# Kernel tuning notes

Hardware: AMD Instinct MI355X
Metric: run time of the kernel (lower is better)

The kernel has to match this reference:

```python
import jax, jax.numpy as jnp
import numpy as np
import math

D_MODEL = 512
N_HEADS = 8
KSIZE = 3
SEQ = 2048
BATCH = 4


def setup_inputs() -> dict:
    key = jax.random.key(0)
    ks = jax.random.split(key, 12)
    f32 = jnp.float32
    scale_in = 1.0 / math.sqrt(D_MODEL)
    inp = {
        "query": jax.random.normal(ks[0], (SEQ, BATCH, D_MODEL), f32),
        "key": jax.random.normal(ks[1], (SEQ, BATCH, D_MODEL), f32),
        "value": jax.random.normal(ks[2], (SEQ, BATCH, D_MODEL), f32),
        # causal mask: 1 where attention allowed (lower triangular), 0 elsewhere
        "attn_mask": jnp.tril(jnp.ones((SEQ, SEQ), jnp.int32)),
        "conv1_w": jax.random.normal(ks[3], (D_MODEL, D_MODEL, KSIZE), f32) * scale_in,
        "conv1_b": jax.random.normal(ks[4], (D_MODEL,), f32) * 0.01,
        "conv2_w": jax.random.normal(ks[5], (D_MODEL, D_MODEL, KSIZE), f32) * scale_in,
        "conv2_b": jax.random.normal(ks[6], (D_MODEL,), f32) * 0.01,
        "lin1_w": jax.random.normal(ks[7], (D_MODEL, D_MODEL), f32) * scale_in,
        "lin1_b": jax.random.normal(ks[8], (D_MODEL,), f32) * 0.01,
        "lin2_w": jax.random.normal(ks[9], (D_MODEL, D_MODEL), f32) * scale_in,
        "lin2_b": jax.random.normal(ks[10], (D_MODEL,), f32) * 0.01,
    }
    return inp


def _causal_conv1d(x, w, b):
    # x: [B, S, C_in]; w: [C_out, C_in, K] (torch Conv1d layout); left-pad K-1 (causal)
    K = w.shape[-1]
    xc = jnp.transpose(x, (0, 2, 1))  # [B, C, S]
    y = jax.lax.conv_general_dilated(
        xc, w, window_strides=(1,), padding=[(K - 1, 0)],
        dimension_numbers=("NCH", "OIH", "NCH"))
    y = y + b[None, :, None]
    return jnp.transpose(y, (0, 2, 1))  # [B, S, C_out]


def reference(query, key, value, attn_mask,
              conv1_w, conv1_b, conv2_w, conv2_b,
              lin1_w, lin1_b, lin2_w, lin2_b):
    h, dk = N_HEADS, D_MODEL // N_HEADS
    S, B, D = query.shape
    q = jnp.transpose(query, (1, 0, 2))  # [B, S, D]
    k = jnp.transpose(key, (1, 0, 2))
    v = jnp.transpose(value, (1, 0, 2))

    q = _causal_conv1d(q, conv1_w, conv1_b).reshape(B, S, h, dk).transpose(0, 2, 1, 3)
    k = _causal_conv1d(k, conv2_w, conv2_b).reshape(B, S, h, dk).transpose(0, 2, 1, 3)
    v = (v @ lin1_w.T + lin1_b).reshape(B, S, h, dk).transpose(0, 2, 1, 3)

    scores = jnp.einsum("bhqd,bhkd->bhqk", q, k) / math.sqrt(dk)
    scores = jnp.where(attn_mask[None, None, :, :] == 0, jnp.float32(-1e9), scores)
    p_attn = jax.nn.softmax(scores, axis=-1)  # dropout p=0.0 (deterministic)
    x = jnp.einsum("bhqk,bhkd->bhqd", p_attn, v)
    x = x.transpose(0, 2, 1, 3).reshape(B, S, D)
    out = x @ lin2_w.T + lin2_b
    return jnp.transpose(out, (1, 0, 2))  # back to [S, B, D]
```

## Files before the change

kernel.cpp:

```cpp
#include <hip/hip_runtime.h>
#include <hip/hip_bf16.h>

#define S_LEN 2048
#define BATCH 4
#define DMODEL 512
#define NHEADS 8
#define DK 64
#define NELEM 4194304
#define WSLOT 786432

typedef __hip_bfloat16 bf16;
typedef unsigned short u16_t;
typedef __attribute__((ext_vector_type(8))) short bfx8;
typedef __attribute__((ext_vector_type(4))) short bfx4;
typedef __attribute__((ext_vector_type(4))) float fx4;

#define MFMA16(a, b, c) __builtin_amdgcn_mfma_f32_16x16x32_bf16(a, b, c, 0, 0, 0)

__device__ __forceinline__ float cvt(float x) { return x; }
__device__ __forceinline__ float cvt(bf16 x) { return __bfloat162float(x); }
__device__ __forceinline__ u16_t f2b(float x) { bf16 h = __float2bfloat16(x); return *(u16_t*)&h; }
__device__ __forceinline__ float b2f16(u16_t u) { bf16 h = *(bf16*)&u; return __bfloat162float(h); }

__global__ void sniff_kernel(const u16_t* __restrict__ q, int* __restrict__ flag) {
    const int lane = threadIdx.x & 63;
    int cnt = 0;
    for (int j = 0; j < 4; j++) {
        int e = (q[2 * (lane + 64 * j)] >> 7) & 0xFF;
        cnt += (int)__popcll(__ballot(e >= 100 && e <= 140));
    }
    if (lane == 0 && blockIdx.x == 0) *flag = (cnt >= 200) ? 1 : 0;
}

__global__ void cvt_in_kernel(const void* __restrict__ q, const void* __restrict__ k,
                              const void* __restrict__ v, u16_t* __restrict__ am,
                              const int* __restrict__ flag) {
    int gid = blockIdx.x * 256 + threadIdx.x;
    int e8 = gid * 8;
    int z = e8 >> 22;
    int off = e8 & (NELEM - 1);
    const void* src = (z == 0) ? q : (z == 1) ? k : v;
    u16_t* dst = am + (size_t)z * NELEM + off;
    if (*flag) {
        *(bfx8*)dst = *(const bfx8*)((const u16_t*)src + off);
    } else {
        const float* s = (const float*)src + off;
        fx4 a = *(const fx4*)s;
        fx4 b = *(const fx4*)(s + 4);
        u16_t tmp[8];
#pragma unroll
        for (int j = 0; j < 4; j++) { tmp[j] = f2b(a[j]); tmp[4 + j] = f2b(b[j]); }
        *(bfx8*)dst = *(const bfx8*)tmp;
    }
}

__global__ void cvt_w_kernel(const void* __restrict__ c1w, const void* __restrict__ c2w,
                             const void* __restrict__ l1w, const void* __restrict__ l2w,
                             const void* __restrict__ b0, const void* __restrict__ b1,
                             const void* __restrict__ b2, const void* __restrict__ b3,
                             u16_t* __restrict__ wt, u16_t* __restrict__ bb,
                             const int* __restrict__ flag) {
    const int isbf = *flag;
    if (blockIdx.x >= 3072) {
        int i = (blockIdx.x - 3072) * 256 + threadIdx.x;
        int p = i >> 9, o = i & 511;
        const void* b = (p == 0) ? b0 : (p == 1) ? b1 : (p == 2) ? b2 : b3;
        bb[i] = f2b(isbf ? cvt(((const bf16*)b)[o]) : ((const float*)b)[o]);
        return;
    }
    int gid = blockIdx.x * 256 + threadIdx.x;
    int e4 = gid * 4;
    int p = e4 / WSLOT;
    int r = e4 - p * WSLOT;
    int t = r >> 18;
    int rem = r & 262143;
    int o = rem >> 9, kk = rem & 511;
    const void* w = (p == 0) ? c1w : (p == 1) ? c2w : (p == 2) ? l1w : l2w;
    u16_t out[4];
#pragma unroll
    for (int j = 0; j < 4; j++) {
        float val;
        if (p < 2) {
            int idx = (o * DMODEL + kk + j) * 3 + t;
            val = isbf ? cvt(((const bf16*)w)[idx]) : ((const float*)w)[idx];
        } else {
            if (t == 2) {
                int idx = o * DMODEL + kk + j;
                val = isbf ? cvt(((const bf16*)w)[idx]) : ((const float*)w)[idx];
            } else val = 0.f;
        }
        out[j] = f2b(val);
    }
    *(bfx4*)(wt + e4) = *(const bfx4*)out;
}

template <int MODE>
__global__ __launch_bounds__(256) void uproj_kernel(
    const u16_t* __restrict__ X, const u16_t* __restrict__ Wt,
    const u16_t* __restrict__ Bb, u16_t* __restrict__ Y,
    void* __restrict__ dout, const int* __restrict__ flag) {
    constexpr int SMEM = (MODE == 0) ? 32832 : 23040;
    __shared__ __align__(16) u16_t smem[SMEM];
    const int tid = threadIdx.x;
    const int wave = tid >> 6, lane = tid & 63;
    const int l16 = lane & 15, quad = lane >> 4;
    const int mb_base = blockIdx.x * 256;
    const int nb_base = blockIdx.y * 64;
    const int z = blockIdx.z;
    const int isconv = (MODE == 0) && (z < 2);
    const u16_t* Xz = X + (size_t)((MODE == 0) ? z : 0) * NELEM;
    const u16_t* Wz = Wt + (size_t)((MODE == 0) ? z : 3) * WSLOT;
    const u16_t* Bz = Bb + ((MODE == 0) ? z : 3) * DMODEL;

    fx4 acc[4][4];
#pragma unroll
    for (int mb = 0; mb < 4; mb++)
#pragma unroll
        for (int nb = 0; nb < 4; nb++) acc[mb][nb] = (fx4){0.f, 0.f, 0.f, 0.f};

    if (isconv) {
        u16_t (*as_)[72] = (u16_t (*)[72])smem;
        u16_t (*ws_)[64][72] = (u16_t (*)[64][72])(smem + 19008);
        bfx8 pa[9], pw[6];
        {
            const int kc = 0;
#pragma unroll
            for (int j = 0; j < 9; j++) {
                int i = tid + 256 * j;
                if (i < 2112) {
                    int r = i >> 3, c8 = (i & 7) << 3;
                    int gm = mb_base - 8 + r;
                    if (gm >= 0) pa[j] = *(const bfx8*)(Xz + (size_t)gm * DMODEL + (kc << 6) + c8);
                    else { bfx8 zv; for (int jj = 0; jj < 8; jj++) zv[jj] = 0; pa[j] = zv; }
                }
            }
#pragma unroll
            for (int j = 0; j < 6; j++) {
                int i = tid + 256 * j;
                int t = i >> 9, rr = (i >> 3) & 63, c8 = (i & 7) << 3;
                pw[j] = *(const bfx8*)(Wz + (size_t)(t * DMODEL + nb_base + rr) * DMODEL + (kc << 6) + c8);
            }
        }
        for (int kc = 0; kc < 8; kc++) {
            __syncthreads();
#pragma unroll
            for (int j = 0; j < 9; j++) {
                int i = tid + 256 * j;
                if (i < 2112) { int r = i >> 3, c8 = (i & 7) << 3; *(bfx8*)&as_[r][c8] = pa[j]; }
            }
#pragma unroll
            for (int j = 0; j < 6; j++) {
                int i = tid + 256 * j;
                int t = i >> 9, rr = (i >> 3) & 63, c8 = (i & 7) << 3;
                *(bfx8*)&ws_[t][rr][c8] = pw[j];
            }
            __syncthreads();
            if (kc < 7) {
                const int kn = kc + 1;
#pragma unroll
                for (int j = 0; j < 9; j++) {
                    int i = tid + 256 * j;
                    if (i < 2112) {
                        int r = i >> 3, c8 = (i & 7) << 3;
                        int gm = mb_base - 8 + r;
                        if (gm >= 0) pa[j] = *(const bfx8*)(Xz + (size_t)gm * DMODEL + (kn << 6) + c8);
                        else { bfx8 zv; for (int jj = 0; jj < 8; jj++) zv[jj] = 0; pa[j] = zv; }
                    }
                }
#pragma unroll
                for (int j = 0; j < 6; j++) {
                    int i = tid + 256 * j;
                    int t = i >> 9, rr = (i >> 3) & 63, c8 = (i & 7) << 3;
                    pw[j] = *(const bfx8*)(Wz + (size_t)(t * DMODEL + nb_base + rr) * DMODEL + (kn << 6) + c8);
                }
            }
#pragma unroll
            for (int c = 0; c < 2; c++) {
#pragma unroll
                for (int t = 0; t < 3; t++) {
                    const int roff = 4 * t;
                    bfx8 av[4];
#pragma unroll
                    for (int mb = 0; mb < 4; mb++)
                        av[mb] = *(const bfx8*)&as_[wave * 64 + mb * 16 + l16 + roff][c * 32 + quad * 8];
#pragma unroll
                    for (int nb = 0; nb < 4; nb++) {
                        bfx8 bfr = *(const bfx8*)&ws_[t][nb * 16 + l16][c * 32 + quad * 8];
#pragma unroll
                        for (int mb = 0; mb < 4; mb++)
                            acc[mb][nb] = MFMA16(av[mb], bfr, acc[mb][nb]);
                    }
                }
            }
        }
    } else {
        u16_t (*as_)[72] = (u16_t (*)[72])smem;
        u16_t (*wsl)[72] = (u16_t (*)[72])(smem + ((MODE == 0) ? 19008 : 18432));
        const u16_t* Wlin = Wz + 2 * (size_t)DMODEL * DMODEL;
        bfx8 pa[8], pw[2];
        {
            const int kc = 0;
#pragma unroll
            for (int j = 0; j < 8; j++) {
                int i = tid + 256 * j;
                int r = i >> 3, c8 = (i & 7) << 3;
                pa[j] = *(const bfx8*)(Xz + (size_t)(mb_base + r) * DMODEL + (kc << 6) + c8);
            }
#pragma unroll
            for (int j = 0; j < 2; j++) {
                int i = tid + 256 * j;
                int rr = i >> 3, c8 = (i & 7) << 3;
                pw[j] = *(const bfx8*)(Wlin + (size_t)(nb_base + rr) * DMODEL + (kc << 6) + c8);
            }
        }
        for (int kc = 0; kc < 8; kc++) {
            __syncthreads();
#pragma unroll
            for (int j = 0; j < 8; j++) {
                int i = tid + 256 * j;
                int r = i >> 3, c8 = (i & 7) << 3;
                *(bfx8*)&as_[r][c8] = pa[j];
            }
#pragma unroll
            for (int j = 0; j < 2; j++) {
                int i = tid + 256 * j;
                int rr = i >> 3, c8 = (i & 7) << 3;
                *(bfx8*)&wsl[rr][c8] = pw[j];
            }
            __syncthreads();
            if (kc < 7) {
                const int kn = kc + 1;
#pragma unroll
                for (int j = 0; j < 8; j++) {
                    int i = tid + 256 * j;
                    int r = i >> 3, c8 = (i & 7) << 3;
                    pa[j] = *(const bfx8*)(Xz + (size_t)(mb_base + r) * DMODEL + (kn << 6) + c8);
                }
#pragma unroll
                for (int j = 0; j < 2; j++) {
                    int i = tid + 256 * j;
                    int rr = i >> 3, c8 = (i & 7) << 3;
                    pw[j] = *(const bfx8*)(Wlin + (size_t)(nb_base + rr) * DMODEL + (kn << 6) + c8);
                }
            }
#pragma unroll
            for (int c = 0; c < 2; c++) {
                bfx8 av[4];
#pragma unroll
                for (int mb = 0; mb < 4; mb++)
                    av[mb] = *(const bfx8*)&as_[wave * 64 + mb * 16 + l16][c * 32 + quad * 8];
#pragma unroll
                for (int nb = 0; nb < 4; nb++) {
                    bfx8 bfr = *(const bfx8*)&wsl[nb * 16 + l16][c * 32 + quad * 8];
#pragma unroll
                    for (int mb = 0; mb < 4; mb++)
                        acc[mb][nb] = MFMA16(av[mb], bfr, acc[mb][nb]);
                }
            }
        }
    }

    const int isbf = *flag;
#pragma unroll
    for (int mb = 0; mb < 4; mb++)
#pragma unroll
        for (int nb = 0; nb < 4; nb++)
#pragma unroll
            for (int r = 0; r < 4; r++) {
                int m = mb_base + wave * 64 + mb * 16 + quad * 4 + r;
                int o = nb_base + nb * 16 + l16;
                float val = acc[mb][nb][r] + b2f16(Bz[o]);
                if (MODE == 0) {
                    int s = m >> 2, b2 = m & 3, h2 = o >> 6, d2 = o & 63;
                    size_t idx = (z == 2)
                        ? (((size_t)(b2 * NHEADS + h2) * DK + d2) * S_LEN + s)
                        : (((size_t)(b2 * NHEADS + h2) * S_LEN + s) * DK + d2);
                    Y[(size_t)z * NELEM + idx] = f2b(val);
                } else {
                    if (isbf) ((bf16*)dout)[(size_t)m * DMODEL + o] = __float2bfloat16(val);
                    else      ((float*)dout)[(size_t)m * DMODEL + o] = val;
                }
            }
}

__global__ __launch_bounds__(256) void mattn_kernel(
    const u16_t* __restrict__ Qp, const u16_t* __restrict__ Kp,
    const u16_t* __restrict__ VpT, u16_t* __restrict__ Out) {
    __shared__ __align__(16) u16_t ks_[64][72];
    __shared__ __align__(16) u16_t vs[64][72];
    __shared__ __align__(16) u16_t ps[4][16][72];
    const int tid = threadIdx.x, wave = tid >> 6, lane = tid & 63;
    const int l16 = lane & 15, quad = lane >> 4;
    const int bh = blockIdx.y;
    const int bb2 = bh >> 3, hh2 = bh & 7;
    const int qts[2] = {(int)blockIdx.x, 31 - (int)blockIdx.x};

    const int r0 = tid >> 3, c8 = (tid & 7) << 3;

    bfx8 qa[2][2];
#pragma unroll
    for (int j = 0; j < 2; j++) {
        const u16_t* qptr = Qp + (bh * S_LEN + (qts[j] << 6) + wave * 16 + l16) * DK + quad * 8;
        qa[j][0] = *(const bfx8*)qptr;
        qa[j][1] = *(const bfx8*)(qptr + 32);
    }
    fx4 o_[2][4];
    float psum[2][4];
#pragma unroll
    for (int j = 0; j < 2; j++) {
#pragma unroll
        for (int nf = 0; nf < 4; nf++) o_[j][nf] = (fx4){0.f, 0.f, 0.f, 0.f};
#pragma unroll
        for (int r = 0; r < 4; r++) psum[j][r] = 0.f;
    }

    bfx8 kf0 = *(const bfx8*)(Kp + (bh * S_LEN + r0) * DK + c8);
    bfx8 kf1 = *(const bfx8*)(Kp + (bh * S_LEN + r0 + 32) * DK + c8);
    bfx8 vf0 = *(const bfx8*)(VpT + (bh * DK + r0) * S_LEN + c8);
    bfx8 vf1 = *(const bfx8*)(VpT + (bh * DK + r0 + 32) * S_LEN + c8);

    const int ktmax = qts[1];
    for (int kt = 0; kt <= ktmax; kt++) {
        const int kbase = kt << 6;
        __syncthreads();
        *(bfx8*)&ks_[r0][c8] = kf0;
        *(bfx8*)&ks_[r0 + 32][c8] = kf1;
        *(bfx8*)&vs[r0][c8] = vf0;
        *(bfx8*)&vs[r0 + 32][c8] = vf1;
        __syncthreads();
        if (kt < ktmax) {
            const int nb = (kt + 1) << 6;
            kf0 = *(const bfx8*)(Kp + (bh * S_LEN + nb + r0) * DK + c8);
            kf1 = *(const bfx8*)(Kp + (bh * S_LEN + nb + r0 + 32) * DK + c8);
            vf0 = *(const bfx8*)(VpT + (bh * DK + r0) * S_LEN + nb + c8);
            vf1 = *(const bfx8*)(VpT + (bh * DK + r0 + 32) * S_LEN + nb + c8);
        }

#pragma unroll
        for (int j = 0; j < 2; j++) {
            if (kt > qts[j]) continue;
            const int qbase = qts[j] << 6;

            fx4 s[4];
#pragma unroll
            for (int nf = 0; nf < 4; nf++) {
                fx4 a = (fx4){0.f, 0.f, 0.f, 0.f};
#pragma unroll
                for (int c = 0; c < 2; c++) {
                    bfx8 bfr = *(const bfx8*)&ks_[nf * 16 + l16][c * 32 + quad * 8];
                    a = MFMA16(qa[j][c], bfr, a);
                }
                s[nf] = a;
            }
            const bool last = (kt == qts[j]);
#pragma unroll
            for (int nf = 0; nf < 4; nf++)
#pragma unroll
                for (int r = 0; r < 4; r++) {
                    float p = __expf(s[nf][r] * 0.125f - 12.0f);
                    if (last) {
                        int kg = kbase + nf * 16 + l16;
                        int qg = qbase + wave * 16 + quad * 4 + r;
                        if (kg > qg) p = 0.f;
                    }
                    s[nf][r] = p;
                }
#pragma unroll
            for (int r = 0; r < 4; r++)
                psum[j][r] += (s[0][r] + s[1][r]) + (s[2][r] + s[3][r]);
#pragma unroll
            for (int nf = 0; nf < 4; nf++)
#pragma unroll
                for (int r = 0; r < 4; r++)
                    ps[wave][quad * 4 + r][nf * 16 + l16] = f2b(s[nf][r]);
            bfx8 pa0 = *(const bfx8*)&ps[wave][l16][quad * 8];
            bfx8 pa1 = *(const bfx8*)&ps[wave][l16][32 + quad * 8];
#pragma unroll
            for (int nf = 0; nf < 4; nf++) {
                bfx8 b0 = *(const bfx8*)&vs[nf * 16 + l16][quad * 8];
                bfx8 b1 = *(const bfx8*)&vs[nf * 16 + l16][32 + quad * 8];
                o_[j][nf] = MFMA16(pa0, b0, o_[j][nf]);
                o_[j][nf] = MFMA16(pa1, b1, o_[j][nf]);
            }
        }
    }

    float l_[2][4];
#pragma unroll
    for (int j = 0; j < 2; j++)
#pragma unroll
        for (int r = 0; r < 4; r++) {
            float v = psum[j][r];
#pragma unroll
            for (int off = 1; off <= 8; off <<= 1) v += __shfl_xor(v, off);
            l_[j][r] = fmaxf(v, 1e-30f);
        }

#pragma unroll
    for (int j = 0; j < 2; j++)
#pragma unroll
        for (int nf = 0; nf < 4; nf++)
#pragma unroll
            for (int r = 0; r < 4; r++) {
                int qg = (qts[j] << 6) + wave * 16 + quad * 4 + r;
                int col = hh2 * 64 + nf * 16 + l16;
                Out[(size_t)(qg * 4 + bb2) * DMODEL + col] =
                    f2b(o_[j][nf][r] / l_[j][r]);
            }
}

extern "C" void kernel_launch(void* const* d_in, const int* in_sizes, int n_in,
                              void* d_out, int out_size, void* d_ws, size_t ws_size,
                              hipStream_t stream) {
    const void* q   = d_in[0];
    const void* k   = d_in[1];
    const void* v   = d_in[2];
    const void* c1w = d_in[4];
    const void* c1b = d_in[5];
    const void* c2w = d_in[6];
    const void* c2b = d_in[7];
    const void* l1w = d_in[8];
    const void* l1b = d_in[9];
    const void* l2w = d_in[10];
    const void* l2b = d_in[11];

    const size_t TEN = (size_t)NELEM * 2;
    char* base = (char*)d_ws;
    int* flag  = (int*)base;
    u16_t* am  = (u16_t*)(base + 512);
    u16_t* qp  = am + 3 * (size_t)NELEM;
    u16_t* kp  = am + 4 * (size_t)NELEM;
    u16_t* vpt = am + 5 * (size_t)NELEM;
    u16_t* wt  = (u16_t*)(base + 512 + 6 * TEN);
    u16_t* bb  = wt + 4 * (size_t)WSLOT;
    u16_t* ctx2 = am;

    sniff_kernel<<<dim3(1), dim3(64), 0, stream>>>((const u16_t*)q, flag);
    cvt_in_kernel<<<dim3(6144), dim3(256), 0, stream>>>(q, k, v, am, flag);
    cvt_w_kernel<<<dim3(3080), dim3(256), 0, stream>>>(c1w, c2w, l1w, l2w,
                                                       c1b, c2b, l1b, l2b, wt, bb, flag);
    uproj_kernel<0><<<dim3(32, 8, 3), dim3(256), 0, stream>>>(am, wt, bb, qp, nullptr, flag);
    mattn_kernel<<<dim3(16, 32), dim3(256), 0, stream>>>(qp, kp, vpt, ctx2);
    uproj_kernel<1><<<dim3(32, 8, 1), dim3(256), 0, stream>>>(ctx2, wt, bb, nullptr, d_out, flag);
}
```

Baseline: 229.5 us.

## Compute transposed attention scores in registers to drop the P shared-memory round trip

The attention kernel now swaps the MFMA operands so S^T is produced directly in the layout needed as the B operand of the PV product. This removes the per-wave shared-memory staging of probabilities. V is written to shared memory with a permuted column order so that it matches. Other changes: K and V fragments are hoisted out of the j loop and shared by both query tiles, exp is replaced by exp2 with a folded scale, the row-sum reduction and output stores are vectorized, and blocks are swizzled across heads. The cost is more complex index mapping, with some risk of mismatched permutations.

```diff
diff --git a/kernel.cpp b/kernel.cpp
--- a/kernel.cpp
+++ b/kernel.cpp
@@ -288,36 +288,41 @@
     const u16_t* __restrict__ VpT, u16_t* __restrict__ Out) {
     __shared__ __align__(16) u16_t ks_[64][72];
     __shared__ __align__(16) u16_t vs[64][72];
-    __shared__ __align__(16) u16_t ps[4][16][72];
     const int tid = threadIdx.x, wave = tid >> 6, lane = tid & 63;
     const int l16 = lane & 15, quad = lane >> 4;
-    const int bh = blockIdx.y;
+    const int flat = (int)blockIdx.y * 16 + (int)blockIdx.x;
+    const int swz = (flat & 7) * 64 + (flat >> 3);
+    const int bh = swz >> 4;
+    const int bx = swz & 15;
     const int bb2 = bh >> 3, hh2 = bh & 7;
-    const int qts[2] = {(int)blockIdx.x, 31 - (int)blockIdx.x};
+    const int qts[2] = {bx, 31 - bx};
 
     const int r0 = tid >> 3, c8 = (tid & 7) << 3;
+    const int pc0 = (c8 & 35) | ((c8 & 16) >> 2) | ((c8 & 12) << 1);
+    const int c84 = c8 + 4;
+    const int pc1 = (c84 & 35) | ((c84 & 16) >> 2) | ((c84 & 12) << 1);
 
     bfx8 qa[2][2];
 #pragma unroll
     for (int j = 0; j < 2; j++) {
-        const u16_t* qptr = Qp + (bh * S_LEN + (qts[j] << 6) + wave * 16 + l16) * DK + quad * 8;
+        const u16_t* qptr = Qp + (size_t)(bh * S_LEN + (qts[j] << 6) + wave * 16 + l16) * DK + quad * 8;
         qa[j][0] = *(const bfx8*)qptr;
         qa[j][1] = *(const bfx8*)(qptr + 32);
     }
     fx4 o_[2][4];
-    float psum[2][4];
-#pragma unroll
-    for (int j = 0; j < 2; j++) {
+    float psum[2] = {0.f, 0.f};
+#pragma unroll
+    for (int j = 0; j < 2; j++)
 #pragma unroll
         for (int nf = 0; nf < 4; nf++) o_[j][nf] = (fx4){0.f, 0.f, 0.f, 0.f};
-#pragma unroll
-        for (int r = 0; r < 4; r++) psum[j][r] = 0.f;
-    }
-
-    bfx8 kf0 = *(const bfx8*)(Kp + (bh * S_LEN + r0) * DK + c8);
-    bfx8 kf1 = *(const bfx8*)(Kp + (bh * S_LEN + r0 + 32) * DK + c8);
-    bfx8 vf0 = *(const bfx8*)(VpT + (bh * DK + r0) * S_LEN + c8);
-    bfx8 vf1 = *(const bfx8*)(VpT + (bh * DK + r0 + 32) * S_LEN + c8);
+
+    bfx8 kf0 = *(const bfx8*)(Kp + (size_t)(bh * S_LEN + r0) * DK + c8);
+    bfx8 kf1 = *(const bfx8*)(Kp + (size_t)(bh * S_LEN + r0 + 32) * DK + c8);
+    bfx8 vf0 = *(const bfx8*)(VpT + (size_t)(bh * DK + r0) * S_LEN + c8);
+    bfx8 vf1 = *(const bfx8*)(VpT + (size_t)(bh * DK + r0 + 32) * S_LEN + c8);
+
+    const int qg0 = (qts[0] << 6) + wave * 16 + l16;
+    const int qg1 = (qts[1] << 6) + wave * 16 + l16;
 
     const int ktmax = qts[1];
     for (int kt = 0; kt <= ktmax; kt++) {
@@ -325,88 +330,103 @@
         __syncthreads();
         *(bfx8*)&ks_[r0][c8] = kf0;
         *(bfx8*)&ks_[r0 + 32][c8] = kf1;
-        *(bfx8*)&vs[r0][c8] = vf0;
-        *(bfx8*)&vs[r0 + 32][c8] = vf1;
+        {
+            bfx4 a0 = {vf0[0], vf0[1], vf0[2], vf0[3]};
+            bfx4 a1 = {vf0[4], vf0[5], vf0[6], vf0[7]};
+            bfx4 b0 = {vf1[0], vf1[1], vf1[2], vf1[3]};
+            bfx4 b1 = {vf1[4], vf1[5], vf1[6], vf1[7]};
+            *(bfx4*)&vs[r0][pc0] = a0;
+            *(bfx4*)&vs[r0][pc1] = a1;
+            *(bfx4*)&vs[r0 + 32][pc0] = b0;
+            *(bfx4*)&vs[r0 + 32][pc1] = b1;
+        }
         __syncthreads();
         if (kt < ktmax) {
             const int nb = (kt + 1) << 6;
-            kf0 = *(const bfx8*)(Kp + (bh * S_LEN + nb + r0) * DK + c8);
-            kf1 = *(const bfx8*)(Kp + (bh * S_LEN + nb + r0 + 32) * DK + c8);
-            vf0 = *(const bfx8*)(VpT + (bh * DK + r0) * S_LEN + nb + c8);
-            vf1 = *(const bfx8*)(VpT + (bh * DK + r0 + 32) * S_LEN + nb + c8);
-        }
-
+            kf0 = *(const bfx8*)(Kp + (size_t)(bh * S_LEN + nb + r0) * DK + c8);
+            kf1 = *(const bfx8*)(Kp + (size_t)(bh * S_LEN + nb + r0 + 32) * DK + c8);
+            vf0 = *(const bfx8*)(VpT + (size_t)(bh * DK + r0) * S_LEN + nb + c8);
+            vf1 = *(const bfx8*)(VpT + (size_t)(bh * DK + r0 + 32) * S_LEN + nb + c8);
+        }
+
+        bfx8 ak[2][4];
+#pragma unroll
+        for (int c = 0; c < 2; c++)
+#pragma unroll
+            for (int nf = 0; nf < 4; nf++)
+                ak[c][nf] = *(const bfx8*)&ks_[nf * 16 + l16][c * 32 + quad * 8];
+
+        bfx8 pb[2][2];
 #pragma unroll
         for (int j = 0; j < 2; j++) {
             if (kt > qts[j]) continue;
-            const int qbase = qts[j] << 6;
-
             fx4 s[4];
 #pragma unroll
             for (int nf = 0; nf < 4; nf++) {
                 fx4 a = (fx4){0.f, 0.f, 0.f, 0.f};
-#pragma unroll
-                for (int c = 0; c < 2; c++) {
-                    bfx8 bfr = *(const bfx8*)&ks_[nf * 16 + l16][c * 32 + quad * 8];
-                    a = MFMA16(qa[j][c], bfr, a);
-                }
+                a = MFMA16(ak[0][nf], qa[j][0], a);
+                a = MFMA16(ak[1][nf], qa[j][1], a);
                 s[nf] = a;
             }
             const bool last = (kt == qts[j]);
+            const int qgj = (j == 0) ? qg0 : qg1;
+            float tsum = 0.f;
+#pragma unroll
+            for (int nf = 0; nf < 4; nf++) {
+                float pr[4];
+#pragma unroll
+                for (int r = 0; r < 4; r++) {
+                    float p = __builtin_amdgcn_exp2f(fmaf(s[nf][r], 0.18033688f, -17.3123405f));
+                    if (last) {
+                        int kg = kbase + nf * 16 + quad * 4 + r;
+                        if (kg > qgj) p = 0.f;
+                    }
+                    pr[r] = p;
+                    pb[j][nf >> 1][(nf & 1) * 4 + r] = (short)f2b(p);
+                }
+                tsum += (pr[0] + pr[1]) + (pr[2] + pr[3]);
+            }
+            psum[j] += tsum;
+        }
+
+        bfx8 av[2][4];
+#pragma unroll
+        for (int c = 0; c < 2; c++)
 #pragma unroll
             for (int nf = 0; nf < 4; nf++)
-#pragma unroll
-                for (int r = 0; r < 4; r++) {
-                    float p = __expf(s[nf][r] * 0.125f - 12.0f);
-                    if (last) {
-                        int kg = kbase + nf * 16 + l16;
-                        int qg = qbase + wave * 16 + quad * 4 + r;
-                        if (kg > qg) p = 0.f;
-                    }
-                    s[nf][r] = p;
-                }
-#pragma unroll
-            for (int r = 0; r < 4; r++)
-                psum[j][r] += (s[0][r] + s[1][r]) + (s[2][r] + s[3][r]);
-#pragma unroll
-            for (int nf = 0; nf < 4; nf++)
-#pragma unroll
-                for (int r = 0; r < 4; r++)
-                    ps[wave][quad * 4 + r][nf * 16 + l16] = f2b(s[nf][r]);
-            bfx8 pa0 = *(const bfx8*)&ps[wave][l16][quad * 8];
-            bfx8 pa1 = *(const bfx8*)&ps[wave][l16][32 + quad * 8];
+                av[c][nf] = *(const bfx8*)&vs[nf * 16 + l16][c * 32 + quad * 8];
+#pragma unroll
+        for (int j = 0; j < 2; j++) {
+            if (kt > qts[j]) continue;
 #pragma unroll
             for (int nf = 0; nf < 4; nf++) {
-                bfx8 b0 = *(const bfx8*)&vs[nf * 16 + l16][quad * 8];
-                bfx8 b1 = *(const bfx8*)&vs[nf * 16 + l16][32 + quad * 8];
-                o_[j][nf] = MFMA16(pa0, b0, o_[j][nf]);
-                o_[j][nf] = MFMA16(pa1, b1, o_[j][nf]);
-            }
-        }
-    }
-
-    float l_[2][4];
-#pragma unroll
-    for (int j = 0; j < 2; j++)
-#pragma unroll
-        for (int r = 0; r < 4; r++) {
-            float v = psum[j][r];
-#pragma unroll
-            for (int off = 1; off <= 8; off <<= 1) v += __shfl_xor(v, off);
-            l_[j][r] = fmaxf(v, 1e-30f);
-        }
-
-#pragma unroll
-    for (int j = 0; j < 2; j++)
-#pragma unroll
-        for (int nf = 0; nf < 4; nf++)
-#pragma unroll
-            for (int r = 0; r < 4; r++) {
-                int qg = (qts[j] << 6) + wave * 16 + quad * 4 + r;
-                int col = hh2 * 64 + nf * 16 + l16;
-                Out[(size_t)(qg * 4 + bb2) * DMODEL + col] =
-                    f2b(o_[j][nf][r] / l_[j][r]);
-            }
+                o_[j][nf] = MFMA16(av[0][nf], pb[j][0], o_[j][nf]);
+                o_[j][nf] = MFMA16(av[1][nf], pb[j][1], o_[j][nf]);
+            }
+        }
+    }
+
+    float l_[2];
+#pragma unroll
+    for (int j = 0; j < 2; j++) {
+        float v = psum[j];
+        v += __shfl_xor(v, 16);
+        v += __shfl_xor(v, 32);
+        l_[j] = fmaxf(v, 1e-30f);
+    }
+
+#pragma unroll
+    for (int j = 0; j < 2; j++) {
+        const float inv = 1.0f / l_[j];
+        const int qg = (j == 0) ? qg0 : qg1;
+#pragma unroll
+        for (int nf = 0; nf < 4; nf++) {
+            bfx4 ov;
+#pragma unroll
+            for (int r = 0; r < 4; r++) ov[r] = (short)f2b(o_[j][nf][r] * inv);
+            *(bfx4*)(Out + (size_t)(qg * 4 + bb2) * DMODEL + hh2 * 64 + nf * 16 + quad * 4) = ov;
+        }
+    }
 }
 
 extern "C" void kernel_launch(void* const* d_in, const int* in_sizes, int n_in,
```

Measured after the change: 224.9 us. -2.0%, faster.
